# Optimization experiments

Hardware: AMD Instinct MI355X
Metric: run time of the kernel (lower is better)

Reference implementation:

```python
import jax, jax.numpy as jnp
import numpy as np

N_HEADS = 4
D_HEAD = 64
SCALE = D_HEAD ** -0.5


def setup_inputs() -> dict:
    key = jax.random.key(0)
    k0, k1, k2, k3, k4 = jax.random.split(key, 5)
    C = 256
    return {
        "x": jax.random.normal(k0, (32, C, 32, 32), dtype=jnp.float32),
        "W_qkv": jax.random.normal(k1, (C, 3 * N_HEADS * D_HEAD), dtype=jnp.float32) * 0.02,
        "b_qkv": jax.random.normal(k2, (3 * N_HEADS * D_HEAD,), dtype=jnp.float32) * 0.02,
        "W_out": jax.random.normal(k3, (C, C), dtype=jnp.float32) * 0.02,
        "b_out": jax.random.normal(k4, (C,), dtype=jnp.float32) * 0.02,
    }


def reference(x, W_qkv, b_qkv, W_out, b_out):
    b, c, h, w = x.shape
    # [B, C, H, W] -> [B, S, C], S = H*W  (NOTE: GroupNorm is defined in the
    # original module but never applied in forward; we match that exactly.)
    xs = x.reshape(b, c, h * w).transpose(0, 2, 1)
    qkv = (xs @ W_qkv + b_qkv).reshape(b, -1, N_HEADS, 3 * D_HEAD)
    q, k, v = jnp.split(qkv, 3, axis=-1)  # each [B, S, H, D]
    scores = jnp.einsum('bihd,bjhd->bijh', q, k) * SCALE  # [B, S, S, H]
    attn = jax.nn.softmax(scores, axis=2)  # softmax over key index j
    res = jnp.einsum('bijh,bjhd->bihd', attn, v).reshape(b, -1, N_HEADS * D_HEAD)
    res = res @ W_out + b_out + xs
    return res.transpose(0, 2, 1).reshape(b, c, h, w)
```

## Files before the change

### kernel.cpp

```cpp
#include <hip/hip_runtime.h>

#define NH 4
#define DH 64
#define SS 1024
#define CC 256

typedef __attribute__((ext_vector_type(8))) short short8;
typedef __attribute__((ext_vector_type(4))) float floatx4;
typedef __attribute__((ext_vector_type(16))) float floatx16;
typedef __attribute__((ext_vector_type(2))) unsigned uint2v;

#define MFMA16(a, b, c) __builtin_amdgcn_mfma_f32_16x16x32_bf16(a, b, c, 0, 0, 0)
#define MFMA32(a, b, c) __builtin_amdgcn_mfma_f32_32x32x16_bf16(a, b, c, 0, 0, 0)

#define QSCALE 0.18033688011112042f

__device__ __forceinline__ short f2bf(float f) {
    union { float f; unsigned u; } v; v.f = f;
    unsigned r = (v.u + 0x7fffu + ((v.u >> 16) & 1u)) >> 16;
    return (short)r;
}
__device__ __forceinline__ unsigned bfrn(float f) {
    union { float f; unsigned u; } v; v.f = f;
    return (v.u + 0x7fffu + ((v.u >> 16) & 1u)) >> 16;
}
__device__ __forceinline__ unsigned pk2_trunc(float a, float b) {
    union { float f; unsigned u; } ua, ub; ua.f = a; ub.f = b;
    return (ua.u >> 16) | (ub.u & 0xFFFF0000u);
}
__device__ __forceinline__ unsigned pk2_rn(float a, float b) {
    return bfrn(a) | (bfrn(b) << 16);
}

__global__ __launch_bounds__(256) void k_prep(const float* __restrict__ x,
                                              const float* __restrict__ Wqkv,
                                              const float* __restrict__ Wout,
                                              short* __restrict__ xs,
                                              short* __restrict__ Wqkv_t,
                                              short* __restrict__ Wout_t) {
    int bid = blockIdx.x;
    if (bid < 2048) {
        __shared__ float tile[64][65];
        int b = bid >> 6;
        int s0 = ((bid >> 2) & 15) * 64;
        int c0 = (bid & 3) * 64;
        int t = threadIdx.x;
        int tx = t & 63, ty = t >> 6;
        for (int i = 0; i < 16; ++i) {
            int c = ty + i * 4;
            tile[tx][c] = x[((b * CC) + (c0 + c)) * SS + s0 + tx];
        }
        __syncthreads();
        for (int i = 0; i < 8; ++i) {
            int s = (t >> 5) + i * 8;
            int cp = (t & 31) * 2;
            short2 v;
            v.x = f2bf(tile[s][cp]);
            v.y = f2bf(tile[s][cp + 1]);
            *(short2*)(&xs[((b * SS) + (s0 + s)) * CC + c0 + cp]) = v;
        }
    } else {
        int idx = (bid - 2048) * 256 + threadIdx.x;
        if (idx < 768 * 256) {
            int n = idx >> 8, k = idx & 255;
            Wqkv_t[idx] = f2bf(Wqkv[k * 768 + n]);
        } else {
            int j = idx - 768 * 256;
            int c = j >> 8, k = j & 255;
            Wout_t[j] = f2bf(Wout[k * 256 + c]);
        }
    }
}

__global__ __launch_bounds__(256) void k_qkv(const short* __restrict__ xs,
                                             const short* __restrict__ Wt,
                                             const float* __restrict__ bqkv,
                                             short* __restrict__ qtw,
                                             short* __restrict__ kw,
                                             short* __restrict__ vtw) {
    __shared__ __align__(16) short smem[10240];
    short* As = smem;
    short* Bs = smem + 4096;
    int bid = blockIdx.x;
    int idx = bid >> 3;
    int m0 = ((bid & 7) * 32 + idx / 6) * 128;
    int n0 = (idx % 6) * 128;
    int t = threadIdx.x;
    int lane = t & 63, wid = t >> 6;
    int wr = wid >> 1, wc = wid & 1;
    int c16 = lane & 15, qd = lane >> 4;

    floatx4 acc[4][4] = {};
    int lrow = lane >> 2, lcol = (lane & 3) * 8;

    for (int kt = 0; kt < 8; ++kt) {
        if (kt) __syncthreads();
#pragma unroll
        for (int j = 0; j < 2; ++j) {
            int r0 = wid * 32 + j * 16;
            const short* ga = xs + (size_t)(m0 + r0 + lrow) * CC + kt * 32 + lcol;
            const short* gb = Wt + (size_t)(n0 + r0 + lrow) * CC + kt * 32 + lcol;
            __builtin_amdgcn_global_load_lds(
                (const __attribute__((address_space(1))) unsigned*)ga,
                (__attribute__((address_space(3))) unsigned*)(As + r0 * 32), 16, 0, 0);
            __builtin_amdgcn_global_load_lds(
                (const __attribute__((address_space(1))) unsigned*)gb,
                (__attribute__((address_space(3))) unsigned*)(Bs + r0 * 32), 16, 0, 0);
        }
        __syncthreads();
        short8 av[4], bv[4];
        for (int i = 0; i < 4; ++i) {
            av[i] = *(const short8*)(&As[(wr * 64 + i * 16 + c16) * 32 + qd * 8]);
            bv[i] = *(const short8*)(&Bs[(wc * 64 + i * 16 + c16) * 32 + qd * 8]);
        }
        for (int mi = 0; mi < 4; ++mi)
            for (int ni = 0; ni < 4; ++ni)
                acc[mi][ni] = MFMA16(av[mi], bv[ni], acc[mi][ni]);
    }

    int b = m0 >> 10, sbase = m0 & 1023;
    int seg = (n0 >> 6) + wc;
    float bias4[4];
    for (int ni = 0; ni < 4; ++ni)
        bias4[ni] = bqkv[n0 + wc * 64 + ni * 16 + c16];

    int seg0 = n0 >> 6;
    short* Tt = smem;
    for (int s2 = 0; s2 < 2; ++s2) {
        int sg = seg0 + s2;
        int type = sg % 3;
        if (type == 1) continue;
        float sc = (type == 0) ? QSCALE : 1.f;
        __syncthreads();
        if (wc == s2) {
            for (int mi = 0; mi < 4; ++mi)
                for (int ni = 0; ni < 4; ++ni)
                    for (int r = 0; r < 4; ++r)
                        Tt[(ni * 16 + c16) * 136 + wr * 64 + mi * 16 + qd * 4 + r] =
                            f2bf((acc[mi][ni][r] + bias4[ni]) * sc);
        }
        __syncthreads();
        short* dst = ((type == 0) ? qtw : vtw) + (size_t)((b * NH + sg / 3) * DH) * SS + sbase;
        for (int it = 0; it < 4; ++it) {
            int c = it * 256 + t;
            int d = c >> 4, off = (c & 15) * 8;
            *(short8*)(dst + (size_t)d * SS + off) =
                *(const short8*)(&Tt[d * 136 + off]);
        }
    }

    int kseg = (seg0 % 3 == 1) ? seg0 : (((seg0 + 1) % 3 == 1) ? seg0 + 1 : -1);
    if (kseg >= 0) {
        short* Kt = smem;
        __syncthreads();
        if (seg == kseg) {
            for (int mi = 0; mi < 4; ++mi)
                for (int ni = 0; ni < 4; ++ni)
                    for (int r = 0; r < 4; ++r)
                        Kt[(wr * 64 + mi * 16 + qd * 4 + r) * 72 + ni * 16 + c16] =
                            f2bf(acc[mi][ni][r] + bias4[ni]);
        }
        __syncthreads();
        int bhk = b * NH + kseg / 3;
        int srow = t >> 1, dh = (t & 1) * 32;
        short* gdst = &kw[(size_t)(bhk * SS + sbase + srow) * DH + dh];
        const short* lsrc = &Kt[srow * 72 + dh];
        for (int k = 0; k < 4; ++k)
            *(short8*)(gdst + k * 8) = *(const short8*)(lsrc + k * 8);
    }
}

__global__ __launch_bounds__(512) void k_attn(const short* __restrict__ qtw,
                                              const short* __restrict__ kw,
                                              const short* __restrict__ vtw,
                                              short* __restrict__ res) {
    __shared__ __align__(16) short Ks[64 * 72];
    __shared__ __align__(16) short Vts[64 * 72];
    int bid = blockIdx.x;
    int q0 = (bid >> 7) * 256;
    int bh = bid & 127;
    int t = threadIdx.x;
    int lane = t & 63, w = t >> 6;
    int l31 = lane & 31, hi = lane >> 5;
    const short* qp = qtw + (size_t)bh * DH * SS;
    const short* kp = kw + (size_t)bh * SS * DH;
    const short* vp = vtw + (size_t)bh * DH * SS;

    short8 qfrag[4];
    {
        int s = q0 + w * 32 + l31;
        for (int kd = 0; kd < 4; ++kd) {
            short8 q;
            for (int e = 0; e < 8; ++e)
                q[e] = qp[(size_t)(kd * 16 + hi * 8 + e) * SS + s];
            qfrag[kd] = q;
        }
    }

    float l_i = 0.f;
    floatx16 o_acc[2] = {};

    int kr = t >> 3, kc = (t & 7) * 8;
    short8 kreg, vreg;
    kreg = *(const short8*)(&kp[kr * DH + kc]);
    vreg = *(const short8*)(&vp[kr * SS + kc]);

    for (int kt = 0; kt < 16; ++kt) {
        if (kt) __syncthreads();
        *(short8*)(&Ks[kr * 72 + kc]) = kreg;
        *(short8*)(&Vts[kr * 72 + kc]) = vreg;
        __syncthreads();
        if (kt < 15) {
            kreg = *(const short8*)(&kp[((kt + 1) * 64 + kr) * DH + kc]);
            vreg = *(const short8*)(&vp[kr * SS + (kt + 1) * 64 + kc]);
        }

#pragma unroll
        for (int jt = 0; jt < 2; ++jt) {
            short8 kf[4];
#pragma unroll
            for (int kd = 0; kd < 4; ++kd)
                kf[kd] = *(const short8*)(&Ks[(jt * 32 + l31) * 72 + kd * 16 + hi * 8]);
            short8 vf0[2], vf1[2];
#pragma unroll
            for (int dt = 0; dt < 2; ++dt) {
                vf0[dt] = *(const short8*)(&Vts[(dt * 32 + l31) * 72 + (jt * 2 + 0) * 16 + hi * 8]);
                vf1[dt] = *(const short8*)(&Vts[(dt * 32 + l31) * 72 + (jt * 2 + 1) * 16 + hi * 8]);
            }

            floatx16 sacc = {};
            __builtin_amdgcn_s_setprio(1);
#pragma unroll
            for (int kd = 0; kd < 4; ++kd)
                sacc = MFMA32(kf[kd], qfrag[kd], sacc);
            __builtin_amdgcn_s_setprio(0);

            float ls = 0.f;
            unsigned u[8];
#pragma unroll
            for (int r = 0; r < 16; r += 2) {
                float e0 = __builtin_amdgcn_exp2f(sacc[r]);
                float e1 = __builtin_amdgcn_exp2f(sacc[r + 1]);
                ls += e0 + e1;
                u[r >> 1] = pk2_trunc(e0, e1);
            }
            l_i += ls;

            uint2v r02 = __builtin_amdgcn_permlane32_swap(u[0], u[2], false, false);
            uint2v r13 = __builtin_amdgcn_permlane32_swap(u[1], u[3], false, false);
            uint2v r46 = __builtin_amdgcn_permlane32_swap(u[4], u[6], false, false);
            uint2v r57 = __builtin_amdgcn_permlane32_swap(u[5], u[7], false, false);
            union { unsigned w[4]; short8 s; } pf0, pf1;
            pf0.w[0] = r02[0]; pf0.w[1] = r13[0]; pf0.w[2] = r02[1]; pf0.w[3] = r13[1];
            pf1.w[0] = r46[0]; pf1.w[1] = r57[0]; pf1.w[2] = r46[1]; pf1.w[3] = r57[1];

            __builtin_amdgcn_s_setprio(1);
#pragma unroll
            for (int dt = 0; dt < 2; ++dt) {
                o_acc[dt] = MFMA32(vf0[dt], pf0.s, o_acc[dt]);
                o_acc[dt] = MFMA32(vf1[dt], pf1.s, o_acc[dt]);
            }
            __builtin_amdgcn_s_setprio(0);
        }
    }

    int b = bh >> 2, h = bh & 3;
    {
        float l = l_i;
        l += __shfl_xor(l, 32);
        float inv = 1.f / l;
        int s = q0 + w * 32 + l31;
        long base = (long)(b * SS + s) * CC + h * DH;
#pragma unroll
        for (int dt = 0; dt < 2; ++dt) {
#pragma unroll
            for (int q = 0; q < 4; ++q) {
                int d = dt * 32 + q * 8 + hi * 4;
                uint2 ow;
                ow.x = pk2_rn(o_acc[dt][q * 4 + 0] * inv, o_acc[dt][q * 4 + 1] * inv);
                ow.y = pk2_rn(o_acc[dt][q * 4 + 2] * inv, o_acc[dt][q * 4 + 3] * inv);
                *(uint2*)(&res[base + d]) = ow;
            }
        }
    }
}

__global__ __launch_bounds__(256) void k_out(const short* __restrict__ res,
                                             const short* __restrict__ Wot,
                                             const float* __restrict__ bout,
                                             const float* __restrict__ x,
                                             float* __restrict__ out) {
    __shared__ short As[2][64 * 40];
    __shared__ short Bs[2][128 * 40];
    int b = blockIdx.z;
    int m0 = blockIdx.y * 64;
    int n0 = blockIdx.x * 128;
    int t = threadIdx.x;
    int lane = t & 63, wid = t >> 6;
    int wr = wid >> 1, wc = wid & 1;
    int c16 = lane & 15, qd = lane >> 4;

    floatx4 acc[2][4] = {};
    int arow = t >> 2, ac4 = (t & 3) * 8;
    int brow0 = t >> 2, bc0 = (t & 3) * 8;
    int brow1 = brow0 + 64;
    short8 pa, pb0, pb1;
    pa  = *(const short8*)(&Wot[(m0 + arow) * CC + ac4]);
    pb0 = *(const short8*)(&res[(b * SS + n0 + brow0) * CC + bc0]);
    pb1 = *(const short8*)(&res[(b * SS + n0 + brow1) * CC + bc0]);
    *(short8*)(&As[0][arow * 40 + ac4]) = pa;
    *(short8*)(&Bs[0][brow0 * 40 + bc0]) = pb0;
    *(short8*)(&Bs[0][brow1 * 40 + bc0]) = pb1;
    __syncthreads();

    int cur = 0;
    for (int kt = 0; kt < 8; ++kt) {
        if (kt < 7) {
            pa  = *(const short8*)(&Wot[(m0 + arow) * CC + (kt + 1) * 32 + ac4]);
            pb0 = *(const short8*)(&res[(b * SS + n0 + brow0) * CC + (kt + 1) * 32 + bc0]);
            pb1 = *(const short8*)(&res[(b * SS + n0 + brow1) * CC + (kt + 1) * 32 + bc0]);
        }
        short8 av[2], bv[4];
        for (int i = 0; i < 2; ++i)
            av[i] = *(const short8*)(&As[cur][(wr * 32 + i * 16 + c16) * 40 + qd * 8]);
        for (int i = 0; i < 4; ++i)
            bv[i] = *(const short8*)(&Bs[cur][(wc * 64 + i * 16 + c16) * 40 + qd * 8]);
        for (int mi = 0; mi < 2; ++mi)
            for (int ni = 0; ni < 4; ++ni)
                acc[mi][ni] = MFMA16(av[mi], bv[ni], acc[mi][ni]);
        if (kt < 7) {
            *(short8*)(&As[cur ^ 1][arow * 40 + ac4]) = pa;
            *(short8*)(&Bs[cur ^ 1][brow0 * 40 + bc0]) = pb0;
            *(short8*)(&Bs[cur ^ 1][brow1 * 40 + bc0]) = pb1;
            __syncthreads();
            cur ^= 1;
        }
    }

    for (int mi = 0; mi < 2; ++mi) {
        for (int r = 0; r < 4; ++r) {
            int c = m0 + wr * 32 + mi * 16 + qd * 4 + r;
            float bias = bout[c];
            for (int ni = 0; ni < 4; ++ni) {
                int s = n0 + wc * 64 + ni * 16 + c16;
                float v = acc[mi][ni][r] + bias + x[((b * CC) + c) * SS + s];
                out[((b * CC) + c) * SS + s] = v;
            }
        }
    }
}

extern "C" void kernel_launch(void* const* d_in, const int* in_sizes, int n_in,
                              void* d_out, int out_size, void* d_ws, size_t ws_size,
                              hipStream_t stream) {
    const float* x    = (const float*)d_in[0];
    const float* Wqkv = (const float*)d_in[1];
    const float* bqkv = (const float*)d_in[2];
    const float* Wout = (const float*)d_in[3];
    const float* bout = (const float*)d_in[4];
    float* out = (float*)d_out;

    char* ws = (char*)d_ws;
    short* xs_res = (short*)(ws);
    short* qtw    = (short*)(ws + 16777216);
    short* kw     = (short*)(ws + 33554432);
    short* vtw    = (short*)(ws + 50331648);
    short* Wqkv_t = (short*)(ws + 67108864);
    short* Wout_t = (short*)(ws + 67502080);

    k_prep<<<dim3(3072), 256, 0, stream>>>(x, Wqkv, Wout, xs_res, Wqkv_t, Wout_t);
    k_qkv<<<dim3(1536), 256, 0, stream>>>(xs_res, Wqkv_t, bqkv, qtw, kw, vtw);
    k_attn<<<dim3(512), 512, 0, stream>>>(qtw, kw, vtw, xs_res);
    k_out<<<dim3(8, 4, 32), 256, 0, stream>>>(xs_res, Wout_t, bout, x, out);
}
```

Before: 170.0 us.

## Split attention key range across wave halves and merge partial sums in LDS

Each attention block now covers 128 queries instead of 256, and its two groups of four waves each process half of the key sequence. Both halves stream their own K/V tiles into separate LDS regions. At the end, the partial outputs and row sums are reduced through shared memory, which works without rescaling because the softmax uses no running max. The grid doubles to 1024 blocks to give the 256 CUs more parallel work, and launch bounds request higher occupancy. The cost is more LDS per block, a final reduction step, and Q loaded twice per block.

```diff
diff --git a/kernel.cpp b/kernel.cpp
--- a/kernel.cpp
+++ b/kernel.cpp
@@ -170,17 +170,17 @@
     }
 }
 
-__global__ __launch_bounds__(512) void k_attn(const short* __restrict__ qtw,
-                                              const short* __restrict__ kw,
-                                              const short* __restrict__ vtw,
-                                              short* __restrict__ res) {
-    __shared__ __align__(16) short Ks[64 * 72];
-    __shared__ __align__(16) short Vts[64 * 72];
+__global__ __launch_bounds__(512, 6) void k_attn(const short* __restrict__ qtw,
+                                                 const short* __restrict__ kw,
+                                                 const short* __restrict__ vtw,
+                                                 short* __restrict__ res) {
+    __shared__ __align__(16) short smem[18432];
     int bid = blockIdx.x;
-    int q0 = (bid >> 7) * 256;
+    int q0 = (bid >> 7) * 128;
     int bh = bid & 127;
     int t = threadIdx.x;
     int lane = t & 63, w = t >> 6;
+    int half = w >> 2, wq = w & 3;
     int l31 = lane & 31, hi = lane >> 5;
     const short* qp = qtw + (size_t)bh * DH * SS;
     const short* kp = kw + (size_t)bh * SS * DH;
@@ -188,7 +188,7 @@
 
     short8 qfrag[4];
     {
-        int s = q0 + w * 32 + l31;
+        int s = q0 + wq * 32 + l31;
         for (int kd = 0; kd < 4; ++kd) {
             short8 q;
             for (int e = 0; e < 8; ++e)
@@ -200,19 +200,28 @@
     float l_i = 0.f;
     floatx16 o_acc[2] = {};
 
+    const short* Kc = smem + half * 9216;
+    const short* Vc = smem + half * 9216 + 4608;
+
     int kr = t >> 3, kc = (t & 7) * 8;
-    short8 kreg, vreg;
-    kreg = *(const short8*)(&kp[kr * DH + kc]);
-    vreg = *(const short8*)(&vp[kr * SS + kc]);
-
-    for (int kt = 0; kt < 16; ++kt) {
-        if (kt) __syncthreads();
-        *(short8*)(&Ks[kr * 72 + kc]) = kreg;
-        *(short8*)(&Vts[kr * 72 + kc]) = vreg;
-        __syncthreads();
-        if (kt < 15) {
-            kreg = *(const short8*)(&kp[((kt + 1) * 64 + kr) * DH + kc]);
-            vreg = *(const short8*)(&vp[kr * SS + (kt + 1) * 64 + kc]);
+    short8 kreg[2], vreg[2];
+    kreg[0] = *(const short8*)(&kp[kr * DH + kc]);
+    vreg[0] = *(const short8*)(&vp[kr * SS + kc]);
+    kreg[1] = *(const short8*)(&kp[(512 + kr) * DH + kc]);
+    vreg[1] = *(const short8*)(&vp[kr * SS + 512 + kc]);
+
+    for (int i = 0; i < 8; ++i) {
+        if (i) __syncthreads();
+        *(short8*)(&smem[kr * 72 + kc]) = kreg[0];
+        *(short8*)(&smem[4608 + kr * 72 + kc]) = vreg[0];
+        *(short8*)(&smem[9216 + kr * 72 + kc]) = kreg[1];
+        *(short8*)(&smem[13824 + kr * 72 + kc]) = vreg[1];
+        __syncthreads();
+        if (i < 7) {
+            kreg[0] = *(const short8*)(&kp[((i + 1) * 64 + kr) * DH + kc]);
+            vreg[0] = *(const short8*)(&vp[kr * SS + (i + 1) * 64 + kc]);
+            kreg[1] = *(const short8*)(&kp[((i + 9) * 64 + kr) * DH + kc]);
+            vreg[1] = *(const short8*)(&vp[kr * SS + (i + 9) * 64 + kc]);
         }
 
 #pragma unroll
@@ -220,12 +229,12 @@
             short8 kf[4];
 #pragma unroll
             for (int kd = 0; kd < 4; ++kd)
-                kf[kd] = *(const short8*)(&Ks[(jt * 32 + l31) * 72 + kd * 16 + hi * 8]);
+                kf[kd] = *(const short8*)(&Kc[(jt * 32 + l31) * 72 + kd * 16 + hi * 8]);
             short8 vf0[2], vf1[2];
 #pragma unroll
             for (int dt = 0; dt < 2; ++dt) {
-                vf0[dt] = *(const short8*)(&Vts[(dt * 32 + l31) * 72 + (jt * 2 + 0) * 16 + hi * 8]);
-                vf1[dt] = *(const short8*)(&Vts[(dt * 32 + l31) * 72 + (jt * 2 + 1) * 16 + hi * 8]);
+                vf0[dt] = *(const short8*)(&Vc[(dt * 32 + l31) * 72 + (jt * 2 + 0) * 16 + hi * 8]);
+                vf1[dt] = *(const short8*)(&Vc[(dt * 32 + l31) * 72 + (jt * 2 + 1) * 16 + hi * 8]);
             }
 
             floatx16 sacc = {};
@@ -264,12 +273,32 @@
         }
     }
 
-    int b = bh >> 2, h = bh & 3;
-    {
+    __syncthreads();
+    float* M = (float*)smem;
+    if (half == 1) {
+        float* row = M + (wq * 64 + lane) * 33;
+#pragma unroll
+        for (int dt = 0; dt < 2; ++dt)
+#pragma unroll
+            for (int r = 0; r < 16; ++r)
+                row[dt * 16 + r] = o_acc[dt][r];
+        row[32] = l_i;
+    }
+    __syncthreads();
+    if (half == 0) {
+        const float* row = M + (wq * 64 + lane) * 33;
+#pragma unroll
+        for (int dt = 0; dt < 2; ++dt)
+#pragma unroll
+            for (int r = 0; r < 16; ++r)
+                o_acc[dt][r] += row[dt * 16 + r];
+        l_i += row[32];
+
+        int b = bh >> 2, h = bh & 3;
         float l = l_i;
         l += __shfl_xor(l, 32);
         float inv = 1.f / l;
-        int s = q0 + w * 32 + l31;
+        int s = q0 + wq * 32 + l31;
         long base = (long)(b * SS + s) * CC + h * DH;
 #pragma unroll
         for (int dt = 0; dt < 2; ++dt) {
@@ -370,6 +399,6 @@
 
     k_prep<<<dim3(3072), 256, 0, stream>>>(x, Wqkv, Wout, xs_res, Wqkv_t, Wout_t);
     k_qkv<<<dim3(1536), 256, 0, stream>>>(xs_res, Wqkv_t, bqkv, qtw, kw, vtw);
-    k_attn<<<dim3(512), 512, 0, stream>>>(qtw, kw, vtw, xs_res);
+    k_attn<<<dim3(1024), 512, 0, stream>>>(qtw, kw, vtw, xs_res);
     k_out<<<dim3(8, 4, 32), 256, 0, stream>>>(xs_res, Wout_t, bout, x, out);
 }
```

After: 644.8 us. 3.79x slower.
